# Kernel optimization log

Hardware: AMD Instinct MI355X
Metric: run time of the kernel (lower is better)

## Reference

```python
import jax, jax.numpy as jnp
import numpy as np

B, S, HALF = 8, 2048, 512
D = 2 * HALF  # input_dim

def setup_inputs() -> dict:
    key = jax.random.key(0)
    ks = jax.random.split(key, 8)
    scale = 1.0 / np.sqrt(D)
    return {
        "t_out": jax.random.normal(ks[0], (B, S, HALF), dtype=jnp.float32),
        "c_out": jax.random.normal(ks[1], (B, S, HALF), dtype=jnp.float32),
        "Wq": jax.random.uniform(ks[2], (D, D), jnp.float32, -scale, scale),
        "bq": jax.random.uniform(ks[3], (D,), jnp.float32, -scale, scale),
        "Wk": jax.random.uniform(ks[4], (D, D), jnp.float32, -scale, scale),
        "bk": jax.random.uniform(ks[5], (D,), jnp.float32, -scale, scale),
        "Wv": jax.random.uniform(ks[6], (D, D), jnp.float32, -scale, scale),
        "bv": jax.random.uniform(ks[7], (D,), jnp.float32, -scale, scale),
    }

def reference(t_out, c_out, Wq, bq, Wk, bk, Wv, bv):
    # combined: [B, S, D]
    combined = jnp.concatenate([t_out, c_out], axis=-1)
    # torch nn.Linear: y = x @ W.T + b
    q = jnp.einsum('bsd,ed->bse', combined, Wq) + bq
    k = jnp.einsum('bsd,ed->bse', combined, Wk) + bk
    v = jnp.einsum('bsd,ed->bse', combined, Wv) + bv
    # Unscaled dot-product attention (no 1/sqrt(d) factor in original)
    scores = jnp.einsum('bqd,bkd->bqk', q, k)  # [B, S, S]
    attn = jax.nn.softmax(scores, axis=-1)
    return jnp.einsum('bqk,bkd->bqd', attn, v)
```

## Files before the change

### kernel.cpp

```cpp
#include <hip/hip_runtime.h>
#include <cstdint>
#include <cstddef>

typedef _Float16 f16;
typedef __attribute__((ext_vector_type(4))) _Float16 f16x4;
typedef __attribute__((ext_vector_type(8))) _Float16 f16x8;
typedef __attribute__((ext_vector_type(4))) float f32x4;

#define MFMA_F16(a, b, c) __builtin_amdgcn_mfma_f32_16x16x32_f16((a), (b), (c), 0, 0, 0)

static constexpr int BB   = 8;
static constexpr int SS   = 2048;
static constexpr int DD   = 1024;
static constexpr int HALF = 512;
static constexpr int TILE = 256 * 32;

__device__ __forceinline__ void gll16(const f16* g, f16* lds) {
  __builtin_amdgcn_global_load_lds(
      (__attribute__((address_space(1))) void*)(g),
      (__attribute__((address_space(3))) void*)(lds), 16, 0, 0);
}

__global__ __launch_bounds__(256) void fused_prep(
    const float* __restrict__ Wq, const float* __restrict__ Wk, const float* __restrict__ Wv,
    const float* __restrict__ t_out, const float* __restrict__ c_out,
    f16* __restrict__ Whq, f16* __restrict__ Whk, f16* __restrict__ Whv,
    f16* __restrict__ Xh)
{
  if (blockIdx.x < 1024) {
    const int i = (blockIdx.x * 256 + threadIdx.x) * 4;
    const float4 q = *(const float4*)(Wq + i);
    const float4 k = *(const float4*)(Wk + i);
    const float4 v = *(const float4*)(Wv + i);
    f16x4 a;
    a.x = (f16)q.x; a.y = (f16)q.y; a.z = (f16)q.z; a.w = (f16)q.w; *(f16x4*)(Whq + i) = a;
    a.x = (f16)k.x; a.y = (f16)k.y; a.z = (f16)k.z; a.w = (f16)k.w; *(f16x4*)(Whk + i) = a;
    a.x = (f16)v.x; a.y = (f16)v.y; a.z = (f16)v.z; a.w = (f16)v.w; *(f16x4*)(Whv + i) = a;
  } else {
    const size_t i = ((size_t)(blockIdx.x - 1024) * 256 + threadIdx.x) * 4;
    const int d = (int)(i & 1023);
    const size_t g = i >> 10;
    const float* src = (d < HALF) ? (t_out + g * HALF + d)
                                  : (c_out + g * HALF + (d - HALF));
    const float4 x = *(const float4*)src;
    f16x4 h;
    h.x = (f16)x.x; h.y = (f16)x.y; h.z = (f16)x.z; h.w = (f16)x.w;
    *(f16x4*)(Xh + i) = h;
  }
}

__device__ __forceinline__ void stage256(
    f16* slot, const f16* g, size_t row0, int ld, int k0, int wave, int lane)
{
#pragma unroll
  for (int q = 0; q < 2; ++q) {
    const int chunk = wave * 128 + q * 64 + lane;
    const int row   = chunk >> 2;
    const int lg    = (chunk & 3) ^ ((row >> 1) & 3);
    gll16(g + (row0 + (size_t)row) * ld + k0 + lg * 8,
          slot + (size_t)(wave * 128 + q * 64) * 8);
  }
}

__device__ __forceinline__ void mma_step(
    const f16* at, const f16* bt, f32x4 acc[8][4],
    int wm, int wn, int col16, int quad)
{
  f16x8 af[8], bf[4];
#pragma unroll
  for (int j = 0; j < 4; ++j) {
    const int r = wn * 64 + j * 16 + col16;
    bf[j] = *(const f16x8*)&bt[r * 32 + ((quad ^ ((r >> 1) & 3)) * 8)];
  }
#pragma unroll
  for (int i = 0; i < 8; ++i) {
    const int r = wm * 128 + i * 16 + col16;
    af[i] = *(const f16x8*)&at[r * 32 + ((quad ^ ((r >> 1) & 3)) * 8)];
  }
  __builtin_amdgcn_s_setprio(1);
#pragma unroll
  for (int i = 0; i < 8; ++i)
#pragma unroll
    for (int j = 0; j < 4; ++j)
      acc[i][j] = MFMA_F16(af[i], bf[j], acc[i][j]);
  __builtin_amdgcn_s_setprio(0);
}

template <int K>
__device__ __forceinline__ void mma_pipeline(
    const f16* __restrict__ A, const f16* __restrict__ B,
    int lda, int ldb, size_t arow0, size_t brow0,
    f16* As, f16* Bs, f32x4 acc[8][4],
    int wave, int lane, int wm, int wn, int col16, int quad)
{
  constexpr int NT = K / 32;
#pragma unroll
  for (int p = 0; p < 3; ++p) {
    stage256(As + p * TILE, A, arow0, lda, p * 32, wave, lane);
    stage256(Bs + p * TILE, B, brow0, ldb, p * 32, wave, lane);
  }
  for (int t = 0; t < NT - 3; ++t) {
    asm volatile("s_waitcnt vmcnt(8)\n\ts_barrier" ::: "memory");
    const int ps = (t + 3) & 3;
    stage256(As + ps * TILE, A, arow0, lda, (t + 3) * 32, wave, lane);
    stage256(Bs + ps * TILE, B, brow0, ldb, (t + 3) * 32, wave, lane);
    const int s = t & 3;
    mma_step(As + s * TILE, Bs + s * TILE, acc, wm, wn, col16, quad);
  }
  asm volatile("s_waitcnt vmcnt(8)\n\ts_barrier" ::: "memory");
  mma_step(As + ((NT - 3) & 3) * TILE, Bs + ((NT - 3) & 3) * TILE, acc, wm, wn, col16, quad);
  asm volatile("s_waitcnt vmcnt(4)\n\ts_barrier" ::: "memory");
  mma_step(As + ((NT - 2) & 3) * TILE, Bs + ((NT - 2) & 3) * TILE, acc, wm, wn, col16, quad);
  asm volatile("s_waitcnt vmcnt(0)\n\ts_barrier" ::: "memory");
  mma_step(As + ((NT - 1) & 3) * TILE, Bs + ((NT - 1) & 3) * TILE, acc, wm, wn, col16, quad);
}

__global__ __launch_bounds__(512, 2) void proj_gemm(
    const f16* __restrict__ Xh,
    const f16* __restrict__ Whq, const f16* __restrict__ Whk, const f16* __restrict__ Whv,
    const float* __restrict__ bq, const float* __restrict__ bk, const float* __restrict__ bv,
    f16* __restrict__ Q, f16* __restrict__ K, f16* __restrict__ Vv)
{
  __shared__ alignas(16) f16 As[4 * TILE];
  __shared__ alignas(16) f16 Bs[4 * TILE];

  const int z = blockIdx.z;
  const f16* Wh = (z == 0) ? Whq : (z == 1) ? Whk : Whv;
  const float* bias = (z == 0) ? bq : (z == 1) ? bk : bv;
  f16* dst = (z == 0) ? Q : (z == 1) ? K : Vv;

  const int t = threadIdx.x, lane = t & 63, wave = t >> 6;
  const int wm = wave >> 2, wn = wave & 3, col16 = lane & 15, quad = lane >> 4;
  const int m0 = blockIdx.x * 256, n0 = blockIdx.y * 256;

  f32x4 acc[8][4];
#pragma unroll
  for (int i = 0; i < 8; ++i)
#pragma unroll
    for (int j = 0; j < 4; ++j) acc[i][j] = f32x4{0.f, 0.f, 0.f, 0.f};

  mma_pipeline<DD>(Xh, Wh, DD, DD, (size_t)m0, (size_t)n0,
                   As, Bs, acc, wave, lane, wm, wn, col16, quad);

#pragma unroll
  for (int j = 0; j < 4; ++j) {
    const int gn = n0 + wn * 64 + j * 16 + col16;
    const float bb_ = bias[gn];
#pragma unroll
    for (int i = 0; i < 8; ++i) {
      const int gm = m0 + wm * 128 + i * 16 + quad * 4;
#pragma unroll
      for (int r = 0; r < 4; ++r)
        dst[(size_t)(gm + r) * DD + gn] = (f16)(acc[i][j][r] + bb_);
    }
  }
}

__global__ __launch_bounds__(256) void transpose_v(
    const f16* __restrict__ Vv, f16* __restrict__ Vt)
{
  __shared__ alignas(16) f16 tile[64][72];
  const int b  = blockIdx.z;
  const int s0 = blockIdx.x * 64;
  const int e0 = blockIdx.y * 64;
  const int t  = threadIdx.x;
  const int r  = t >> 3;
  const int c8 = (t & 7) * 8;

  const f16* src0 = Vv + ((size_t)(b * SS + s0 + r)) * DD + e0 + c8;
  const f16* src1 = Vv + ((size_t)(b * SS + s0 + r + 32)) * DD + e0 + c8;
  *(int4*)&tile[r][c8]      = *(const int4*)src0;
  *(int4*)&tile[r + 32][c8] = *(const int4*)src1;
  __syncthreads();

  f16x8 v0, v1;
#pragma unroll
  for (int u = 0; u < 8; ++u) {
    v0[u] = tile[c8 + u][r];
    v1[u] = tile[c8 + u][r + 32];
  }
  f16* dst0 = Vt + ((size_t)b * DD + e0 + r) * SS + s0 + c8;
  f16* dst1 = Vt + ((size_t)b * DD + e0 + r + 32) * SS + s0 + c8;
  *(f16x8*)dst0 = v0;
  *(f16x8*)dst1 = v1;
}

__global__ __launch_bounds__(512, 2) void qk_gemm(
    const f16* __restrict__ Q, const f16* __restrict__ K, f16* __restrict__ Sc,
    int b0)
{
  __shared__ alignas(16) f16 As[4 * TILE];
  __shared__ alignas(16) f16 Bs[4 * TILE];

  const int bb = blockIdx.z;
  const int t = threadIdx.x, lane = t & 63, wave = t >> 6;
  const int wm = wave >> 2, wn = wave & 3, col16 = lane & 15, quad = lane >> 4;
  const int m0 = blockIdx.y * 256, n0 = blockIdx.x * 256;

  const size_t arow0 = (size_t)(b0 + bb) * SS + m0;
  const size_t brow0 = (size_t)(b0 + bb) * SS + n0;

  f32x4 acc[8][4];
#pragma unroll
  for (int i = 0; i < 8; ++i)
#pragma unroll
    for (int j = 0; j < 4; ++j) acc[i][j] = f32x4{0.f, 0.f, 0.f, 0.f};

  mma_pipeline<DD>(Q, K, DD, DD, arow0, brow0,
                   As, Bs, acc, wave, lane, wm, wn, col16, quad);

#pragma unroll
  for (int i = 0; i < 8; ++i)
#pragma unroll
    for (int j = 0; j < 4; ++j)
#pragma unroll
      for (int r = 0; r < 4; ++r) {
        const int gm = m0 + wm * 128 + i * 16 + quad * 4 + r;
        const int gn = n0 + wn * 64 + j * 16 + col16;
        Sc[((size_t)bb * SS + gm) * SS + gn] = (f16)acc[i][j][r];
      }
}

__global__ __launch_bounds__(256) void softmax_rows(f16* __restrict__ Sc)
{
  const size_t row = blockIdx.x;
  f16* p = Sc + row * SS;
  const int t = threadIdx.x;

  const f16x8 v = *(const f16x8*)(p + t * 8);
  float xs[8];
#pragma unroll
  for (int u = 0; u < 8; ++u) xs[u] = (float)v[u];

  float m = xs[0];
#pragma unroll
  for (int u = 1; u < 8; ++u) m = fmaxf(m, xs[u]);
#pragma unroll
  for (int off = 32; off > 0; off >>= 1) m = fmaxf(m, __shfl_xor(m, off));
  __shared__ float redm[4];
  __shared__ float reds[4];
  if ((t & 63) == 0) redm[t >> 6] = m;
  __syncthreads();
  m = fmaxf(fmaxf(redm[0], redm[1]), fmaxf(redm[2], redm[3]));

  float e[8];
  float s = 0.f;
#pragma unroll
  for (int u = 0; u < 8; ++u) {
    e[u] = expf(xs[u] - m);
    s += e[u];
  }
#pragma unroll
  for (int off = 32; off > 0; off >>= 1) s += __shfl_xor(s, off);
  if ((t & 63) == 0) reds[t >> 6] = s;
  __syncthreads();
  s = reds[0] + reds[1] + reds[2] + reds[3];
  const float inv = 1.0f / s;

  f16x8 o;
#pragma unroll
  for (int u = 0; u < 8; ++u) o[u] = (f16)(e[u] * inv);
  *(f16x8*)(p + t * 8) = o;
}

__global__ __launch_bounds__(512, 2) void pv_gemm(
    const f16* __restrict__ P, const f16* __restrict__ Vt, float* __restrict__ out,
    int b0)
{
  __shared__ alignas(16) f16 As[4 * TILE];
  __shared__ alignas(16) f16 Bs[4 * TILE];

  const int bb = blockIdx.z;
  const int t = threadIdx.x, lane = t & 63, wave = t >> 6;
  const int wm = wave >> 2, wn = wave & 3, col16 = lane & 15, quad = lane >> 4;
  const int m0 = blockIdx.y * 256;
  const int n0 = blockIdx.x * 256;

  const size_t arow0 = (size_t)bb * SS + m0;
  const size_t brow0 = (size_t)(b0 + bb) * DD + n0;

  f32x4 acc[8][4];
#pragma unroll
  for (int i = 0; i < 8; ++i)
#pragma unroll
    for (int j = 0; j < 4; ++j) acc[i][j] = f32x4{0.f, 0.f, 0.f, 0.f};

  mma_pipeline<SS>(P, Vt, SS, SS, arow0, brow0,
                   As, Bs, acc, wave, lane, wm, wn, col16, quad);

#pragma unroll
  for (int i = 0; i < 8; ++i)
#pragma unroll
    for (int j = 0; j < 4; ++j)
#pragma unroll
      for (int r = 0; r < 4; ++r) {
        const int gm = m0 + wm * 128 + i * 16 + quad * 4 + r;
        const int gn = n0 + wn * 64 + j * 16 + col16;
        out[((size_t)(b0 + bb) * SS + gm) * DD + gn] = acc[i][j][r];
      }
}

extern "C" void kernel_launch(void* const* d_in, const int* in_sizes, int n_in,
                              void* d_out, int out_size, void* d_ws, size_t ws_size,
                              hipStream_t stream)
{
  const float* t_out = (const float*)d_in[0];
  const float* c_out = (const float*)d_in[1];
  const float* Wq    = (const float*)d_in[2];
  const float* bq    = (const float*)d_in[3];
  const float* Wk    = (const float*)d_in[4];
  const float* bk    = (const float*)d_in[5];
  const float* Wv    = (const float*)d_in[6];
  const float* bv    = (const float*)d_in[7];
  float* out = (float*)d_out;

  const size_t WELT  = (size_t)DD * DD;
  const size_t TD8   = (size_t)BB * SS * DD;
  const size_t XH_B  = TD8 * sizeof(f16);
  const size_t SC1_B = (size_t)SS * SS * sizeof(f16);

  const size_t FIXED = 3 * WELT * sizeof(f16) + 4 * XH_B;
  int c = 2;
  for (int cand : {8, 4}) {
    size_t xsc = (size_t)cand * SC1_B;
    if (xsc < XH_B) xsc = XH_B;
    if (FIXED + xsc <= ws_size) { c = cand; break; }
  }
  size_t xsc_bytes = (size_t)c * SC1_B;
  if (xsc_bytes < XH_B) xsc_bytes = XH_B;

  char* ws = (char*)d_ws;
  f16* Whq = (f16*)ws;
  f16* Whk = Whq + WELT;
  f16* Whv = Whk + WELT;
  char* XSc = (char*)(Whv + WELT);
  f16* Xh = (f16*)XSc;
  f16* Sc = (f16*)XSc;
  f16* Q  = (f16*)(XSc + xsc_bytes);
  f16* K  = Q  + TD8;
  f16* Vv = K  + TD8;
  f16* Vt = Vv + TD8;

  fused_prep<<<dim3(1024 + 16384), dim3(256), 0, stream>>>(
      Wq, Wk, Wv, t_out, c_out, Whq, Whk, Whv, Xh);
  proj_gemm<<<dim3(64, 4, 3), dim3(512), 0, stream>>>(
      Xh, Whq, Whk, Whv, bq, bk, bv, Q, K, Vv);
  transpose_v<<<dim3(32, 16, 8), dim3(256), 0, stream>>>(Vv, Vt);

  for (int b0 = 0; b0 < BB; b0 += c) {
    qk_gemm<<<dim3(8, 8, c), dim3(512), 0, stream>>>(Q, K, Sc, b0);
    softmax_rows<<<dim3(c * SS), dim3(256), 0, stream>>>(Sc);
    pv_gemm<<<dim3(4, 8, c), dim3(512), 0, stream>>>(Sc, Vt, out, b0);
  }
}
```

Baseline: 488.1 us.

## Split GEMM k-step into two half phases with specialized A/B staging waves

Restructures the shared GEMM main loop so each k-tile is processed in two halves of the A rows, each preceded by a barrier and issuing half of the next tile's global-to-LDS loads. Waves 0-3 now stage A and waves 4-7 stage B instead of every wave loading both. The intent is to interleave loads and MFMA more finely and to cut the A fragment registers held at once from 8 to 4, easing register pressure. In exchange it doubles the number of barriers per k-step, and the vmcnt counts must still match the new per-wave load count.

```diff
diff --git a/kernel.cpp b/kernel.cpp
--- a/kernel.cpp
+++ b/kernel.cpp
@@ -13,7 +13,7 @@
 static constexpr int SS   = 2048;
 static constexpr int DD   = 1024;
 static constexpr int HALF = 512;
-static constexpr int TILE = 256 * 32;
+static constexpr int T32  = 256 * 32;
 
 __device__ __forceinline__ void gll16(const f16* g, f16* lds) {
   __builtin_amdgcn_global_load_lds(
@@ -49,41 +49,16 @@
   }
 }
 
-__device__ __forceinline__ void stage256(
-    f16* slot, const f16* g, size_t row0, int ld, int k0, int wave, int lane)
+__device__ __forceinline__ void stage_half(
+    f16* s, const f16* g, size_t r0, int ld, int k0, int u, int w4, int rr, int gg)
 {
 #pragma unroll
   for (int q = 0; q < 2; ++q) {
-    const int chunk = wave * 128 + q * 64 + lane;
-    const int row   = chunk >> 2;
-    const int lg    = (chunk & 3) ^ ((row >> 1) & 3);
-    gll16(g + (row0 + (size_t)row) * ld + k0 + lg * 8,
-          slot + (size_t)(wave * 128 + q * 64) * 8);
-  }
-}
-
-__device__ __forceinline__ void mma_step(
-    const f16* at, const f16* bt, f32x4 acc[8][4],
-    int wm, int wn, int col16, int quad)
-{
-  f16x8 af[8], bf[4];
-#pragma unroll
-  for (int j = 0; j < 4; ++j) {
-    const int r = wn * 64 + j * 16 + col16;
-    bf[j] = *(const f16x8*)&bt[r * 32 + ((quad ^ ((r >> 1) & 3)) * 8)];
-  }
-#pragma unroll
-  for (int i = 0; i < 8; ++i) {
-    const int r = wm * 128 + i * 16 + col16;
-    af[i] = *(const f16x8*)&at[r * 32 + ((quad ^ ((r >> 1) & 3)) * 8)];
-  }
-  __builtin_amdgcn_s_setprio(1);
-#pragma unroll
-  for (int i = 0; i < 8; ++i)
-#pragma unroll
-    for (int j = 0; j < 4; ++j)
-      acc[i][j] = MFMA_F16(af[i], bf[j], acc[i][j]);
-  __builtin_amdgcn_s_setprio(0);
+    const int rb  = u * 128 + w4 * 32 + q * 16;
+    const int row = rb + rr;
+    const int lg  = gg ^ ((row >> 1) & 3);
+    gll16(g + (r0 + (size_t)row) * ld + k0 + lg * 8, s + (size_t)rb * 32);
+  }
 }
 
 template <int K>
@@ -94,25 +69,66 @@
     int wave, int lane, int wm, int wn, int col16, int quad)
 {
   constexpr int NT = K / 32;
-#pragma unroll
-  for (int p = 0; p < 3; ++p) {
-    stage256(As + p * TILE, A, arow0, lda, p * 32, wave, lane);
-    stage256(Bs + p * TILE, B, brow0, ldb, p * 32, wave, lane);
-  }
-  for (int t = 0; t < NT - 3; ++t) {
-    asm volatile("s_waitcnt vmcnt(8)\n\ts_barrier" ::: "memory");
-    const int ps = (t + 3) & 3;
-    stage256(As + ps * TILE, A, arow0, lda, (t + 3) * 32, wave, lane);
-    stage256(Bs + ps * TILE, B, brow0, ldb, (t + 3) * 32, wave, lane);
-    const int s = t & 3;
-    mma_step(As + s * TILE, Bs + s * TILE, acc, wm, wn, col16, quad);
-  }
-  asm volatile("s_waitcnt vmcnt(8)\n\ts_barrier" ::: "memory");
-  mma_step(As + ((NT - 3) & 3) * TILE, Bs + ((NT - 3) & 3) * TILE, acc, wm, wn, col16, quad);
-  asm volatile("s_waitcnt vmcnt(4)\n\ts_barrier" ::: "memory");
-  mma_step(As + ((NT - 2) & 3) * TILE, Bs + ((NT - 2) & 3) * TILE, acc, wm, wn, col16, quad);
-  asm volatile("s_waitcnt vmcnt(0)\n\ts_barrier" ::: "memory");
-  mma_step(As + ((NT - 1) & 3) * TILE, Bs + ((NT - 1) & 3) * TILE, acc, wm, wn, col16, quad);
+  const int w4 = wave & 3, rr = lane >> 2, gg = lane & 3;
+  const f16*  g_st  = (wave < 4) ? A : B;
+  const size_t r0_st = (wave < 4) ? arow0 : brow0;
+  const int    ld_st = (wave < 4) ? lda : ldb;
+  f16*         ring  = (wave < 4) ? As : Bs;
+
+#pragma unroll
+  for (int pt = 0; pt < 3; ++pt)
+#pragma unroll
+    for (int u = 0; u < 2; ++u)
+      stage_half(ring + pt * T32, g_st, r0_st, ld_st, pt * 32, u, w4, rr, gg);
+
+  for (int t = 0; t < NT; ++t) {
+    const f16* At = As + (t & 3) * T32;
+    const f16* Bt = Bs + (t & 3) * T32;
+    f16* Sn = ring + ((t + 3) & 3) * T32;
+    const bool st = (t + 3 < NT);
+    const int kn = (t + 3) * 32;
+
+    f16x8 a[4], b[4];
+
+    if (t < NT - 2)       asm volatile("s_waitcnt vmcnt(8)\n\ts_barrier" ::: "memory");
+    else if (t == NT - 2) asm volatile("s_waitcnt vmcnt(4)\n\ts_barrier" ::: "memory");
+    else                  asm volatile("s_waitcnt vmcnt(0)\n\ts_barrier" ::: "memory");
+    if (st) stage_half(Sn, g_st, r0_st, ld_st, kn, 0, w4, rr, gg);
+#pragma unroll
+    for (int j = 0; j < 4; ++j) {
+      const int r = wn * 64 + j * 16 + col16;
+      b[j] = *(const f16x8*)&Bt[r * 32 + ((quad ^ ((r >> 1) & 3)) << 3)];
+    }
+#pragma unroll
+    for (int i = 0; i < 4; ++i) {
+      const int r = wm * 128 + i * 16 + col16;
+      a[i] = *(const f16x8*)&At[r * 32 + ((quad ^ ((r >> 1) & 3)) << 3)];
+    }
+    __builtin_amdgcn_s_setprio(1);
+#pragma unroll
+    for (int i = 0; i < 4; ++i)
+#pragma unroll
+      for (int j = 0; j < 4; ++j)
+        acc[i][j] = MFMA_F16(a[i], b[j], acc[i][j]);
+    __builtin_amdgcn_s_setprio(0);
+
+    if (t < NT - 2)       asm volatile("s_waitcnt vmcnt(8)\n\ts_barrier" ::: "memory");
+    else if (t == NT - 2) asm volatile("s_waitcnt vmcnt(4)\n\ts_barrier" ::: "memory");
+    else                  asm volatile("s_waitcnt vmcnt(0)\n\ts_barrier" ::: "memory");
+    if (st) stage_half(Sn, g_st, r0_st, ld_st, kn, 1, w4, rr, gg);
+#pragma unroll
+    for (int i = 0; i < 4; ++i) {
+      const int r = wm * 128 + 64 + i * 16 + col16;
+      a[i] = *(const f16x8*)&At[r * 32 + ((quad ^ ((r >> 1) & 3)) << 3)];
+    }
+    __builtin_amdgcn_s_setprio(1);
+#pragma unroll
+    for (int i = 0; i < 4; ++i)
+#pragma unroll
+      for (int j = 0; j < 4; ++j)
+        acc[i + 4][j] = MFMA_F16(a[i], b[j], acc[i + 4][j]);
+    __builtin_amdgcn_s_setprio(0);
+  }
 }
 
 __global__ __launch_bounds__(512, 2) void proj_gemm(
@@ -121,8 +137,8 @@
     const float* __restrict__ bq, const float* __restrict__ bk, const float* __restrict__ bv,
     f16* __restrict__ Q, f16* __restrict__ K, f16* __restrict__ Vv)
 {
-  __shared__ alignas(16) f16 As[4 * TILE];
-  __shared__ alignas(16) f16 Bs[4 * TILE];
+  __shared__ alignas(16) f16 As[4 * T32];
+  __shared__ alignas(16) f16 Bs[4 * T32];
 
   const int z = blockIdx.z;
   const f16* Wh = (z == 0) ? Whq : (z == 1) ? Whk : Whv;
@@ -189,8 +205,8 @@
     const f16* __restrict__ Q, const f16* __restrict__ K, f16* __restrict__ Sc,
     int b0)
 {
-  __shared__ alignas(16) f16 As[4 * TILE];
-  __shared__ alignas(16) f16 Bs[4 * TILE];
+  __shared__ alignas(16) f16 As[4 * T32];
+  __shared__ alignas(16) f16 Bs[4 * T32];
 
   const int bb = blockIdx.z;
   const int t = threadIdx.x, lane = t & 63, wave = t >> 6;
@@ -267,8 +283,8 @@
     const f16* __restrict__ P, const f16* __restrict__ Vt, float* __restrict__ out,
     int b0)
 {
-  __shared__ alignas(16) f16 As[4 * TILE];
-  __shared__ alignas(16) f16 Bs[4 * TILE];
+  __shared__ alignas(16) f16 As[4 * T32];
+  __shared__ alignas(16) f16 Bs[4 * T32];
 
   const int bb = blockIdx.z;
   const int t = threadIdx.x, lane = t & 63, wave = t >> 6;
```

Result: faster. 437.3 us (-10.4%).
